# Kernel tuning notes

Hardware: AMD Instinct MI355X
Metric: run time of the kernel (lower is better)

## Reference

```python
import jax, jax.numpy as jnp
import numpy as np

B, S, E, H, W, L = 2048, 50, 256, 512, 256, 50  # batch, seq, emb, hidden, weight, answer_seq_len
V = 50 + 1  # input_size + 1 embedding rows


def _uni(k, shape, bound):
    return jax.random.uniform(k, shape, jnp.float32, -bound, bound)


def setup_inputs() -> dict:
    key = jax.random.key(0)
    ks = jax.random.split(key, 14)
    kb = 1.0 / np.sqrt(H)  # torch LSTM/Linear init bound 1/sqrt(hidden)
    inp = {
        'input': jax.random.randint(ks[0], (B, S), 0, V),
        'emb': jax.random.normal(ks[1], (V, E), jnp.float32),
        'enc_Wih': _uni(ks[2], (4 * H, E), kb),
        'enc_Whh': _uni(ks[3], (4 * H, H), kb),
        'enc_bih': _uni(ks[4], (4 * H,), kb),
        'enc_bhh': _uni(ks[5], (4 * H,), kb),
        'dec_Wih': _uni(ks[6], (4 * H, E), kb),
        'dec_Whh': _uni(ks[7], (4 * H, H), kb),
        'dec_bih': _uni(ks[8], (4 * H,), kb),
        'dec_bhh': _uni(ks[9], (4 * H,), kb),
        'W1': _uni(ks[10], (W, H), kb),
        'W2': _uni(ks[11], (W, H), kb),
        'vt': _uni(ks[12], (W,), 1.0 / np.sqrt(W)),
    }
    return inp


def _lstm_cell(x, h, c, Wih, Whh, bih, bhh):
    gates = x @ Wih.T + h @ Whh.T + (bih + bhh)
    i, f, g, o = jnp.split(gates, 4, axis=-1)  # torch gate order i,f,g,o
    c = jax.nn.sigmoid(f) * c + jax.nn.sigmoid(i) * jnp.tanh(g)
    h = jax.nn.sigmoid(o) * jnp.tanh(c)
    return h, c


def reference(input, emb, enc_Wih, enc_Whh, enc_bih, enc_bhh,
              dec_Wih, dec_Whh, dec_bih, dec_bhh, W1, W2, vt):
    x = emb[input]  # [B,S,E]

    def enc_step(carry, xt):
        h, c = carry
        h, c = _lstm_cell(xt, h, c, enc_Wih, enc_Whh, enc_bih, enc_bhh)
        return (h, c), h

    z = jnp.zeros((B, H), x.dtype)
    _, enc_seq = jax.lax.scan(enc_step, (z, z), x.transpose(1, 0, 2))  # [S,B,H]
    enc_states = enc_seq.transpose(1, 0, 2)  # [B,S,H]

    # W1(encoder_states) is loop-invariant; compute once (same math as per-step recompute)
    blend1 = jnp.einsum('bsh,wh->bsw', enc_states, W1)  # [B,S,W]

    dec_in = jnp.zeros((B, E), x.dtype)  # original never updates decoder_input
    h0 = jnp.zeros((B, H), x.dtype)
    c0 = enc_seq[-1]  # cell_state = encoder_states[-1]
    mask0 = jnp.zeros((B, S), bool)

    def dec_step(carry, k):
        h, c, mask = carry
        h, c = _lstm_cell(dec_in, h, c, dec_Wih, dec_Whh, dec_bih, dec_bhh)
        blend2 = h @ W2.T  # [B,W]
        scores = jnp.einsum('bsw,w->bs', jnp.tanh(blend1 + blend2[:, None, :]), vt)
        scores = jnp.where(mask, jnp.float32(-100000.0), scores)
        logp = jax.nn.log_softmax(scores, axis=-1)  # [B,S]
        chosen = jax.random.categorical(k, logp, axis=-1)  # [B]
        mask = mask.at[jnp.arange(B), chosen].set(True)
        return (h, c, mask), (logp, chosen)

    keys = jax.random.split(jax.random.key(42), L)
    _, (probs, tour) = jax.lax.scan(dec_step, (h0, c0, mask0), keys)
    probs = probs.transpose(1, 0, 2)  # [B,L,S]
    tour = tour.transpose(1, 0)       # [B,L]
    return probs, tour
```

## Files before the change

kernel.cpp:

```cpp
#include <hip/hip_runtime.h>
#include <cstdint>

#define Bsz 2048
#define Ssz 50
#define Esz 256
#define Hsz 512
#define Wsz 256
#define Lsz 50
#define Vsz 51
#define KI 16
#define CH 5
#define GFRAGC2 ((size_t)32 * 128 * 512)

#define JAX_THREEFRY_PARTITIONABLE 1

typedef _Float16 f16;
typedef _Float16 f16x8 __attribute__((ext_vector_type(8)));
typedef float f32x4 __attribute__((ext_vector_type(4)));

__host__ __device__ __forceinline__ void threefry2x32_hd(
    unsigned k0, unsigned k1, unsigned x0, unsigned x1,
    unsigned& o0, unsigned& o1) {
  unsigned ks2 = k0 ^ k1 ^ 0x1BD11BDAu;
  x0 += k0; x1 += k1;
#define TF_RND(r) { x0 += x1; x1 = (x1 << (r)) | (x1 >> (32 - (r))); x1 ^= x0; }
  TF_RND(13) TF_RND(15) TF_RND(26) TF_RND(6)
  x0 += k1; x1 += ks2 + 1u;
  TF_RND(17) TF_RND(29) TF_RND(16) TF_RND(24)
  x0 += ks2; x1 += k0 + 2u;
  TF_RND(13) TF_RND(15) TF_RND(26) TF_RND(6)
  x0 += k0; x1 += k1 + 3u;
  TF_RND(17) TF_RND(29) TF_RND(16) TF_RND(24)
  x0 += k1; x1 += ks2 + 4u;
  TF_RND(13) TF_RND(15) TF_RND(26) TF_RND(6)
  x0 += ks2; x1 += k0 + 5u;
#undef TF_RND
  o0 = x0; o1 = x1;
}

__global__ __launch_bounds__(512) void prep_gfrag(const float* __restrict__ Whh,
                                                  f16* __restrict__ dst) {
  int blk = blockIdx.x;
  int ntile = blk >> 5, kc = blk & 31;
  int t = threadIdx.x;
  int l = t >> 3, e = t & 7;
  int c = l & 15, kg = l >> 4;
  int n = ntile * 16 + c;
  int k = (kc & 15) * 32 + kg * 8 + e;
  int j = n >> 2, g = n & 3;
  float w = Whh[(size_t)(g * 512 + j) * 512 + k];
  f16 hi = (f16)w;
  float lo = w - (float)hi;
  f16 val = (kc < 16) ? hi : (f16)(lo * 2048.0f);
  dst[((size_t)kc * 128 + ntile) * 512 + t] = val;
}

__global__ __launch_bounds__(512) void prep_bfrag(const float* __restrict__ Wm,
                                                  f16* __restrict__ dst) {
  int blk = blockIdx.x;
  int wtile = blk >> 5, kc = blk & 31;
  int t = threadIdx.x;
  int l = t >> 3, e = t & 7;
  int c = l & 15, kg = l >> 4;
  int n = wtile * 16 + c;
  int k = (kc & 15) * 32 + kg * 8 + e;
  float w = Wm[(size_t)n * 512 + k];
  f16 hi = (f16)w;
  float lo = w - (float)hi;
  f16 val = (kc < 16) ? hi : (f16)(lo * 2048.0f);
  dst[((size_t)kc * 16 + wtile) * 512 + t] = val;
}

__global__ __launch_bounds__(256) void prep_encin(
    const float* __restrict__ emb, const float* __restrict__ Wih,
    const float* __restrict__ bih, const float* __restrict__ bhh,
    float* __restrict__ encInP) {
  int wid = blockIdx.x * 4 + (threadIdx.x >> 6);
  int lane = threadIdx.x & 63;
  if (wid >= Vsz * 2048) return;
  int v = wid >> 11, col = wid & 2047;
  float4 e = ((const float4*)emb)[v * 64 + lane];
  float4 w = ((const float4*)Wih)[col * 64 + lane];
  float d = e.x * w.x + e.y * w.y + e.z * w.z + e.w * w.w;
  for (int off = 32; off; off >>= 1) d += __shfl_xor(d, off);
  if (lane == 0) {
    int g = col >> 9, j = col & 511;
    encInP[(size_t)v * 2048 + j * 4 + g] = d + bih[col] + bhh[col];
  }
}

__global__ __launch_bounds__(256) void prep_dbias(const float* __restrict__ a,
                                                  const float* __restrict__ b,
                                                  float* __restrict__ dst) {
  int col = blockIdx.x * 256 + threadIdx.x;
  int g = col >> 9, j = col & 511;
  dst[j * 4 + g] = a[col] + b[col];
}

__global__ __launch_bounds__(256, 2) void gates_mfma(
    const f16* __restrict__ Afrag,
    const f16* __restrict__ Bfrag,
    const float* __restrict__ addtab, const int* __restrict__ input, int tstep,
    f16* __restrict__ Aout,
    float* __restrict__ cio) {
  __shared__ float Cst[64][132];
  const int t = threadIdx.x;
  const int lane = t & 63;
  const int wid = t >> 6;
  const int wm = wid >> 1, wn = wid & 1;
  const int bid = blockIdx.x;
  const int xcd = bid & 7, loc = bid >> 3;
  const int mblk = xcd * 4 + (loc >> 4);
  const int nblk = loc & 15;

  const f16* Ab = Afrag + (size_t)(mblk * 4 + wm * 2) * 512 + lane * 8;
  const f16* Bb = Bfrag + (size_t)(nblk * 8 + wn * 4) * 512 + lane * 8;

  f32x4 acc1[2][4], acc2[2][4];
  {
    f32x4 z = {0.f, 0.f, 0.f, 0.f};
#pragma unroll
    for (int i = 0; i < 2; ++i)
#pragma unroll
      for (int j = 0; j < 4; ++j) { acc1[i][j] = z; acc2[i][j] = z; }
  }

  f16x8 pah[2], pal[2], pbh[4], pbl[4];
  f16x8 qah[2], qal[2], qbh[4], qbl[4];

#define GLOAD(AH_, AL_, BH_, BL_, ki_)                                        \
  {                                                                           \
    const f16* ak = Ab + (size_t)(ki_)*65536;                                 \
    const f16* bk = Bb + (size_t)(ki_)*65536;                                 \
    _Pragma("unroll")                                                         \
    for (int q = 0; q < 2; ++q) {                                             \
      AH_[q] = *(const f16x8*)(ak + q * 512);                                 \
      AL_[q] = *(const f16x8*)(ak + (size_t)16 * 65536 + q * 512);            \
    }                                                                         \
    _Pragma("unroll")                                                         \
    for (int q = 0; q < 4; ++q) {                                             \
      BH_[q] = *(const f16x8*)(bk + q * 512);                                 \
      BL_[q] = *(const f16x8*)(bk + (size_t)16 * 65536 + q * 512);            \
    }                                                                         \
  }
#define GMM(AH_, AL_, BH_, BL_)                                               \
  {                                                                           \
    _Pragma("unroll")                                                         \
    for (int mt = 0; mt < 2; ++mt)                                            \
      _Pragma("unroll")                                                       \
      for (int nt = 0; nt < 4; ++nt)                                          \
        acc1[mt][nt] = __builtin_amdgcn_mfma_f32_16x16x32_f16(                \
            AH_[mt], BH_[nt], acc1[mt][nt], 0, 0, 0);                         \
    _Pragma("unroll")                                                         \
    for (int mt = 0; mt < 2; ++mt)                                            \
      _Pragma("unroll")                                                       \
      for (int nt = 0; nt < 4; ++nt)                                          \
        acc1[mt][nt] = __builtin_amdgcn_mfma_f32_16x16x32_f16(                \
            AL_[mt], BH_[nt], acc1[mt][nt], 0, 0, 0);                         \
    _Pragma("unroll")                                                         \
    for (int mt = 0; mt < 2; ++mt)                                            \
      _Pragma("unroll")                                                       \
      for (int nt = 0; nt < 4; ++nt)                                          \
        acc2[mt][nt] = __builtin_amdgcn_mfma_f32_16x16x32_f16(                \
            AH_[mt], BL_[nt], acc2[mt][nt], 0, 0, 0);                         \
  }

  GLOAD(pah, pal, pbh, pbl, 0)
#pragma unroll 1
  for (int ki = 0; ki < KI; ki += 2) {
    GLOAD(qah, qal, qbh, qbl, ki + 1)
    GMM(pah, pal, pbh, pbl)
    if (ki + 2 < KI) GLOAD(pah, pal, pbh, pbl, ki + 2)
    GMM(qah, qal, qbh, qbl)
  }
#undef GLOAD
#undef GMM

#pragma unroll
  for (int mt = 0; mt < 2; ++mt)
#pragma unroll
    for (int nt = 0; nt < 4; ++nt)
#pragma unroll
      for (int rg = 0; rg < 4; ++rg)
        Cst[wm * 32 + mt * 16 + (lane >> 4) * 4 + rg]
           [wn * 64 + nt * 16 + (lane & 15)] =
            acc1[mt][nt][rg] + acc2[mt][nt][rg] * (1.0f / 2048.0f);
  __syncthreads();

  const int bloc = t & 63, jg = t >> 6;
  const int bg = mblk * 64 + bloc;
  const float* arow = input
      ? addtab + (size_t)input[(size_t)bg * Ssz + tstep] * 2048
      : addtab;

  const int j0 = nblk * 32 + jg * 8;
  float* cp = cio + (size_t)bg * 512 + j0;
  float4 cv0 = *(const float4*)(cp);
  float4 cv1 = *(const float4*)(cp + 4);
  float cin[8] = {cv0.x, cv0.y, cv0.z, cv0.w, cv1.x, cv1.y, cv1.z, cv1.w};
  float cn[8], hv[8];
#pragma unroll
  for (int jj = 0; jj < 8; ++jj) {
    float4 gq = *(const float4*)(&Cst[bloc][jg * 32 + jj * 4]);
    float4 av = *(const float4*)(arow + (size_t)(j0 + jj) * 4);
    float gi = gq.x + av.x;
    float gf = gq.y + av.y;
    float gg = gq.z + av.z;
    float go = gq.w + av.w;
    float si = 1.0f / (1.0f + expf(-gi));
    float sf = 1.0f / (1.0f + expf(-gf));
    float sg = tanhf(gg);
    float so = 1.0f / (1.0f + expf(-go));
    float c2 = sf * cin[jj] + si * sg;
    cn[jj] = c2;
    hv[jj] = so * tanhf(c2);
  }
  *(float4*)(cp)     = make_float4(cn[0], cn[1], cn[2], cn[3]);
  *(float4*)(cp + 4) = make_float4(cn[4], cn[5], cn[6], cn[7]);

  f16x8 hi8, lo8;
#pragma unroll
  for (int jj = 0; jj < 8; ++jj) {
    f16 hi = (f16)hv[jj];
    hi8[jj] = hi;
    lo8[jj] = (f16)(hv[jj] - (float)hi);
  }
  const int kcH = j0 >> 5;
  const int kg = (j0 >> 3) & 3;
  size_t base = (((size_t)kcH * 128 + (bg >> 4)) * 64 + kg * 16 + (bg & 15)) * 8;
  *(f16x8*)(Aout + base)                       = hi8;
  *(f16x8*)(Aout + base + (size_t)16 * 65536)  = lo8;
}

__global__ __launch_bounds__(256) void blend_big(
    const f16* __restrict__ hChunk, const f16* __restrict__ Wb,
    float* __restrict__ outBase, int stepStride, int rowStride) {
  const int t = threadIdx.x, lane = t & 63, wid = t >> 6;
  const int wm = wid >> 1, wn = wid & 1;
  const int bid = blockIdx.x;
  const int nblk = bid / (CH * 32);
  const int mblkG = bid % (CH * 32);
  const int s = mblkG >> 5;
  const int mblkL = mblkG & 31;
  const f16* Ab = hChunk + (size_t)s * GFRAGC2
                + (size_t)(mblkL * 4 + wm * 2) * 512 + lane * 8;
  const f16* Bb = Wb + (size_t)(nblk * 2 + wn) * 512 + lane * 8;

  f32x4 acc1[2], acc2[2];
  {
    f32x4 z = {0.f, 0.f, 0.f, 0.f};
    acc1[0] = z; acc1[1] = z; acc2[0] = z; acc2[1] = z;
  }
  f16x8 pah[2], pal[2], pbh, pbl, qah[2], qal[2], qbh, qbl;

#define BLOAD(AH_, AL_, BH_, BL_, ki_)                                        \
  {                                                                           \
    const f16* ak = Ab + (size_t)(ki_)*65536;                                 \
    const f16* bk = Bb + (size_t)(ki_)*8192;                                  \
    _Pragma("unroll")                                                         \
    for (int q = 0; q < 2; ++q) {                                             \
      AH_[q] = *(const f16x8*)(ak + q * 512);                                 \
      AL_[q] = *(const f16x8*)(ak + (size_t)16 * 65536 + q * 512);            \
    }                                                                         \
    BH_ = *(const f16x8*)(bk);                                                \
    BL_ = *(const f16x8*)(bk + (size_t)16 * 8192);                            \
  }
#define BMM(AH_, AL_, BH_, BL_)                                               \
  {                                                                           \
    _Pragma("unroll")                                                         \
    for (int mt = 0; mt < 2; ++mt)                                            \
      acc1[mt] = __builtin_amdgcn_mfma_f32_16x16x32_f16(                      \
          AH_[mt], BH_, acc1[mt], 0, 0, 0);                                   \
    _Pragma("unroll")                                                         \
    for (int mt = 0; mt < 2; ++mt)                                            \
      acc1[mt] = __builtin_amdgcn_mfma_f32_16x16x32_f16(                      \
          AL_[mt], BH_, acc1[mt], 0, 0, 0);                                   \
    _Pragma("unroll")                                                         \
    for (int mt = 0; mt < 2; ++mt)                                            \
      acc2[mt] = __builtin_amdgcn_mfma_f32_16x16x32_f16(                      \
          AH_[mt], BL_, acc2[mt], 0, 0, 0);                                   \
  }

  BLOAD(pah, pal, pbh, pbl, 0)
#pragma unroll 1
  for (int ki = 0; ki < KI; ki += 2) {
    BLOAD(qah, qal, qbh, qbl, ki + 1)
    BMM(pah, pal, pbh, pbl)
    if (ki + 2 < KI) BLOAD(pah, pal, pbh, pbl, ki + 2)
    BMM(qah, qal, qbh, qbl)
  }
#undef BLOAD
#undef BMM

  const int r = lane & 15, rg4 = (lane >> 4) * 4;
  float* ob = outBase + (size_t)s * stepStride;
#pragma unroll
  for (int mt = 0; mt < 2; ++mt)
#pragma unroll
    for (int rg = 0; rg < 4; ++rg) {
      int b = mblkL * 64 + wm * 32 + mt * 16 + rg4 + rg;
      int w = nblk * 32 + wn * 16 + r;
      ob[(size_t)b * rowStride + w] = acc1[mt][rg] + acc2[mt][rg] * (1.0f / 2048.0f);
    }
}

__global__ __launch_bounds__(256) void dec_cinit(const f16* __restrict__ hE,
                                                 float* __restrict__ cD) {
  int idx = blockIdx.x * 256 + threadIdx.x;
  int b = idx >> 9, j = idx & 511;
  size_t base = (((size_t)(j >> 5) * 128 + (b >> 4)) * 64
                 + ((j >> 3) & 3) * 16 + (b & 15)) * 8 + (j & 7);
  cD[idx] = (float)hE[base] + (float)hE[base + (size_t)16 * 65536];
}

__global__ __launch_bounds__(256) void scores_sample(
    const float* __restrict__ b1, const float* __restrict__ b2,
    const float* __restrict__ vt, unsigned long long* __restrict__ mask,
    float* __restrict__ probs, float* __restrict__ tour,
    int stepk, unsigned kA, unsigned kB) {
  __shared__ float b2s[256];
  __shared__ float vts[256];
  __shared__ float sc[52];
  const int t = threadIdx.x, b = blockIdx.x;
  b2s[t] = b2[(size_t)b * Wsz + t];
  vts[t] = vt[t];
  __syncthreads();
  const int wave = t >> 6, lane = t & 63;
  for (int s = wave; s < Ssz; s += 4) {
    const float* row = b1 + ((size_t)b * Ssz + s) * Wsz;
    float v = 0.f;
#pragma unroll
    for (int q = 0; q < 4; ++q) {
      int w = lane + 64 * q;
      v += vts[w] * tanhf(row[w] + b2s[w]);
    }
    for (int off = 32; off; off >>= 1) v += __shfl_xor(v, off);
    if (lane == 0) sc[s] = v;
  }
  __syncthreads();
  if (wave == 0) {
    unsigned long long m = mask[b];
    float x = (lane < Ssz) ? sc[lane] : -INFINITY;
    if (lane < Ssz && ((m >> lane) & 1ull)) x = -100000.0f;
    float mv = x;
    for (int off = 32; off; off >>= 1) mv = fmaxf(mv, __shfl_xor(mv, off));
    float sh = x - mv;
    float e = (lane < Ssz) ? expf(sh) : 0.f;
    float ssum = e;
    for (int off = 32; off; off >>= 1) ssum += __shfl_xor(ssum, off);
    float lg = logf(ssum);
    float logp = sh - lg;
    if (lane < Ssz) probs[(size_t)b * (Lsz * Ssz) + stepk * Ssz + lane] = logp;

    float val = -INFINITY;
    if (lane < Ssz) {
      unsigned j = (unsigned)(b * Ssz + lane);
      unsigned o0, o1, bits;
#if JAX_THREEFRY_PARTITIONABLE
      threefry2x32_hd(kA, kB, 0u, j, o0, o1);
      bits = o0 ^ o1;
#else
      if (j < 51200u) { threefry2x32_hd(kA, kB, j, j + 51200u, o0, o1); bits = o0; }
      else           { threefry2x32_hd(kA, kB, j - 51200u, j, o0, o1); bits = o1; }
#endif
      float f = __uint_as_float((bits >> 9) | 0x3F800000u) - 1.0f;
      float u = fmaxf(1.17549435e-38f, f + 1.17549435e-38f);
      val = logp - logf(-logf(u));
    }
    int idx = lane;
    for (int off = 32; off; off >>= 1) {
      float ov = __shfl_xor(val, off);
      int oi = __shfl_xor(idx, off);
      if (ov > val || (ov == val && oi < idx)) { val = ov; idx = oi; }
    }
    if (lane == 0) {
      tour[(size_t)b * Lsz + stepk] = (float)idx;
      mask[b] = m | (1ull << idx);
    }
  }
}

extern "C" void kernel_launch(void* const* d_in, const int* in_sizes, int n_in,
                              void* d_out, int out_size, void* d_ws, size_t ws_size,
                              hipStream_t stream) {
  (void)in_sizes; (void)n_in; (void)out_size; (void)ws_size;
  const int*   input = (const int*)d_in[0];
  const float* emb   = (const float*)d_in[1];
  const float* eWih  = (const float*)d_in[2];
  const float* eWhh  = (const float*)d_in[3];
  const float* ebih  = (const float*)d_in[4];
  const float* ebhh  = (const float*)d_in[5];
  const float* dWhh  = (const float*)d_in[7];
  const float* dbih  = (const float*)d_in[8];
  const float* dbhh  = (const float*)d_in[9];
  const float* W1    = (const float*)d_in[10];
  const float* W2    = (const float*)d_in[11];
  const float* vt    = (const float*)d_in[12];
  float* outF = (float*)d_out;

  float* wsf = (float*)d_ws;
  size_t o = 0;
  const size_t BFRAG = (size_t)32 * 16 * 512;
  f16* BfE = (f16*)(wsf + o); o += GFRAGC2 / 2;
  f16* BfD = (f16*)(wsf + o); o += GFRAGC2 / 2;
  f16* Bb1 = (f16*)(wsf + o); o += BFRAG / 2;
  f16* Bb2 = (f16*)(wsf + o); o += BFRAG / 2;
  float* encInP = wsf + o; o += (size_t)Vsz * 2048;
  float* dbiasP = wsf + o; o += 2048;
  f16* hZero = (f16*)(wsf + o); o += GFRAGC2 / 2;
  f16* hBuf  = (f16*)(wsf + o); o += CH * (GFRAGC2 / 2);
  float* cE  = wsf + o; o += (size_t)Bsz * Hsz;
  float* b2c = wsf + o; o += (size_t)CH * Bsz * Wsz;
  float* b1  = wsf + o; o += (size_t)Bsz * Ssz * Wsz;
  unsigned long long* maskp = (unsigned long long*)(wsf + o); o += Bsz * 2;

  hipMemsetAsync(hZero, 0, GFRAGC2 * 2, stream);
  hipMemsetAsync(cE, 0, (size_t)Bsz * Hsz * 4, stream);
  hipMemsetAsync(maskp, 0, (size_t)Bsz * 8, stream);

  prep_gfrag<<<128 * 32, 512, 0, stream>>>(eWhh, BfE);
  prep_gfrag<<<128 * 32, 512, 0, stream>>>(dWhh, BfD);
  prep_bfrag<<<16 * 32, 512, 0, stream>>>(W1, Bb1);
  prep_bfrag<<<16 * 32, 512, 0, stream>>>(W2, Bb2);
  prep_encin<<<(Vsz * 2048) / 4, 256, 0, stream>>>(emb, eWih, ebih, ebhh, encInP);
  prep_dbias<<<8, 256, 0, stream>>>(dbih, dbhh, dbiasP);

  unsigned kAh[Lsz], kBh[Lsz];
  for (int k = 0; k < Lsz; ++k) {
#if JAX_THREEFRY_PARTITIONABLE
    threefry2x32_hd(0u, 42u, 0u, (unsigned)k, kAh[k], kBh[k]);
#else
    unsigned a0, a1, c0, c1;
    if (k < 25) {
      threefry2x32_hd(0u, 42u, 2u * k,      2u * k + 50u, a0, a1); kAh[k] = a0;
      threefry2x32_hd(0u, 42u, 2u * k + 1u, 2u * k + 51u, c0, c1); kBh[k] = c0;
    } else {
      threefry2x32_hd(0u, 42u, 2u * k - 50u, 2u * k,      a0, a1); kAh[k] = a1;
      threefry2x32_hd(0u, 42u, 2u * k - 49u, 2u * k + 1u, c0, c1); kBh[k] = c1;
    }
#endif
  }

  const size_t GF = GFRAGC2;

  for (int c = 0; c < Ssz / CH; ++c) {
    for (int s = 0; s < CH; ++s) {
      int t = c * CH + s;
      const f16* in = (t == 0) ? hZero : hBuf + (size_t)((t - 1) % CH) * GF;
      gates_mfma<<<512, 256, 0, stream>>>(in, BfE, encInP, input, t,
                                          hBuf + (size_t)s * GF, cE);
    }
    blend_big<<<8 * CH * 32, 256, 0, stream>>>(hBuf, Bb1,
                                               b1 + (size_t)(c * CH) * Wsz,
                                               Wsz, Ssz * Wsz);
  }
  dec_cinit<<<(Bsz * Hsz) / 256, 256, 0, stream>>>(
      hBuf + (size_t)((Ssz - 1) % CH) * GF, cE);

  for (int c = 0; c < Lsz / CH; ++c) {
    for (int s = 0; s < CH; ++s) {
      int k = c * CH + s;
      const f16* in = (k == 0) ? hZero : hBuf + (size_t)((k - 1) % CH) * GF;
      gates_mfma<<<512, 256, 0, stream>>>(in, BfD, dbiasP, nullptr, 0,
                                          hBuf + (size_t)s * GF, cE);
    }
    blend_big<<<8 * CH * 32, 256, 0, stream>>>(hBuf, Bb2, b2c,
                                               Bsz * Wsz, Wsz);
    for (int s = 0; s < CH; ++s) {
      int k = c * CH + s;
      scores_sample<<<Bsz, 256, 0, stream>>>(b1, b2c + (size_t)s * Bsz * Wsz,
                                             vt, maskp, outF,
                                             outF + (size_t)Bsz * Lsz * Ssz,
                                             k, kAh[k], kBh[k]);
    }
  }
}
```

Measured before the change: 3.923 ms.

## Fuse per-step sampling into chunked kernel with LDS-cached blend1, enlarge chunk

Replaces the per-step scores_sample launches with one sample_chunk kernel per chunk. It loads each batch row's blend1 (50x256 floats, 51 KB) into LDS once and loops over the chunk's decode steps, keeping the mask in a register and computing the threefry step keys on device. CH doubles from 5 to 10, halving the blend_big launches and growing the workspace buffers. blend_big's block index mapping is reordered so blocks sharing an M-tile land on the same XCD. The large LDS allocation limits occupancy of the sampling kernel.

```diff
diff --git a/kernel.cpp b/kernel.cpp
--- a/kernel.cpp
+++ b/kernel.cpp
@@ -9,7 +9,7 @@
 #define Lsz 50
 #define Vsz 51
 #define KI 16
-#define CH 5
+#define CH 10
 #define GFRAGC2 ((size_t)32 * 128 * 512)
 
 #define JAX_THREEFRY_PARTITIONABLE 1
@@ -238,10 +238,13 @@
   const int t = threadIdx.x, lane = t & 63, wid = t >> 6;
   const int wm = wid >> 1, wn = wid & 1;
   const int bid = blockIdx.x;
-  const int nblk = bid / (CH * 32);
-  const int mblkG = bid % (CH * 32);
-  const int s = mblkG >> 5;
-  const int mblkL = mblkG & 31;
+  const int xcd = bid & 7;
+  const int r1 = bid >> 3;
+  const int nblk = r1 & 7;
+  const int r2 = r1 >> 3;
+  const int mrem = r2 & 3;
+  const int s = r2 >> 2;
+  const int mblkL = xcd * 4 + mrem;
   const f16* Ab = hChunk + (size_t)s * GFRAGC2
                 + (size_t)(mblkL * 4 + wm * 2) * 512 + lane * 8;
   const f16* Bb = Wb + (size_t)(nblk * 2 + wn) * 512 + lane * 8;
@@ -313,71 +316,96 @@
   cD[idx] = (float)hE[base] + (float)hE[base + (size_t)16 * 65536];
 }
 
-__global__ __launch_bounds__(256) void scores_sample(
-    const float* __restrict__ b1, const float* __restrict__ b2,
+__global__ __launch_bounds__(256) void sample_chunk(
+    const float* __restrict__ b1, const float* __restrict__ b2c,
     const float* __restrict__ vt, unsigned long long* __restrict__ mask,
-    float* __restrict__ probs, float* __restrict__ tour,
-    int stepk, unsigned kA, unsigned kB) {
-  __shared__ float b2s[256];
-  __shared__ float vts[256];
+    float* __restrict__ probs, float* __restrict__ tour, int k0) {
+  __shared__ float b1s[Ssz * Wsz];
+  __shared__ float b2s[Wsz];
+  __shared__ float vts[Wsz];
   __shared__ float sc[52];
   const int t = threadIdx.x, b = blockIdx.x;
-  b2s[t] = b2[(size_t)b * Wsz + t];
   vts[t] = vt[t];
-  __syncthreads();
+  {
+    const float4* src = (const float4*)(b1 + (size_t)b * Ssz * Wsz);
+    for (int i = t; i < (Ssz * Wsz) / 4; i += 256)
+      ((float4*)b1s)[i] = src[i];
+  }
+  unsigned long long m = mask[b];
   const int wave = t >> 6, lane = t & 63;
-  for (int s = wave; s < Ssz; s += 4) {
-    const float* row = b1 + ((size_t)b * Ssz + s) * Wsz;
-    float v = 0.f;
-#pragma unroll
-    for (int q = 0; q < 4; ++q) {
-      int w = lane + 64 * q;
-      v += vts[w] * tanhf(row[w] + b2s[w]);
+
+  for (int kk = 0; kk < CH; ++kk) {
+    const int stepk = k0 + kk;
+    __syncthreads();
+    b2s[t] = b2c[((size_t)kk * Bsz + b) * Wsz + t];
+    __syncthreads();
+    for (int s = wave; s < Ssz; s += 4) {
+      const float* row = b1s + s * Wsz;
+      float v = 0.f;
+#pragma unroll
+      for (int q = 0; q < 4; ++q) {
+        int w = lane + 64 * q;
+        v += vts[w] * tanhf(row[w] + b2s[w]);
+      }
+      for (int off = 32; off; off >>= 1) v += __shfl_xor(v, off);
+      if (lane == 0) sc[s] = v;
     }
-    for (int off = 32; off; off >>= 1) v += __shfl_xor(v, off);
-    if (lane == 0) sc[s] = v;
-  }
-  __syncthreads();
-  if (wave == 0) {
-    unsigned long long m = mask[b];
-    float x = (lane < Ssz) ? sc[lane] : -INFINITY;
-    if (lane < Ssz && ((m >> lane) & 1ull)) x = -100000.0f;
-    float mv = x;
-    for (int off = 32; off; off >>= 1) mv = fmaxf(mv, __shfl_xor(mv, off));
-    float sh = x - mv;
-    float e = (lane < Ssz) ? expf(sh) : 0.f;
-    float ssum = e;
-    for (int off = 32; off; off >>= 1) ssum += __shfl_xor(ssum, off);
-    float lg = logf(ssum);
-    float logp = sh - lg;
-    if (lane < Ssz) probs[(size_t)b * (Lsz * Ssz) + stepk * Ssz + lane] = logp;
-
-    float val = -INFINITY;
-    if (lane < Ssz) {
-      unsigned j = (unsigned)(b * Ssz + lane);
-      unsigned o0, o1, bits;
+    __syncthreads();
+    if (wave == 0) {
+      float x = (lane < Ssz) ? sc[lane] : -INFINITY;
+      if (lane < Ssz && ((m >> lane) & 1ull)) x = -100000.0f;
+      float mv = x;
+      for (int off = 32; off; off >>= 1) mv = fmaxf(mv, __shfl_xor(mv, off));
+      float sh = x - mv;
+      float e = (lane < Ssz) ? expf(sh) : 0.f;
+      float ssum = e;
+      for (int off = 32; off; off >>= 1) ssum += __shfl_xor(ssum, off);
+      float lg = logf(ssum);
+      float logp = sh - lg;
+      if (lane < Ssz) probs[(size_t)b * (Lsz * Ssz) + stepk * Ssz + lane] = logp;
+
+      unsigned kA, kB;
 #if JAX_THREEFRY_PARTITIONABLE
-      threefry2x32_hd(kA, kB, 0u, j, o0, o1);
-      bits = o0 ^ o1;
+      threefry2x32_hd(0u, 42u, 0u, (unsigned)stepk, kA, kB);
 #else
-      if (j < 51200u) { threefry2x32_hd(kA, kB, j, j + 51200u, o0, o1); bits = o0; }
-      else           { threefry2x32_hd(kA, kB, j - 51200u, j, o0, o1); bits = o1; }
+      {
+        unsigned a0, a1, c0, c1;
+        int k = stepk;
+        if (k < 25) {
+          threefry2x32_hd(0u, 42u, 2u * k,      2u * k + 50u, a0, a1); kA = a0;
+          threefry2x32_hd(0u, 42u, 2u * k + 1u, 2u * k + 51u, c0, c1); kB = c0;
+        } else {
+          threefry2x32_hd(0u, 42u, 2u * k - 50u, 2u * k,      a0, a1); kA = a1;
+          threefry2x32_hd(0u, 42u, 2u * k - 49u, 2u * k + 1u, c0, c1); kB = c1;
+        }
+      }
 #endif
-      float f = __uint_as_float((bits >> 9) | 0x3F800000u) - 1.0f;
-      float u = fmaxf(1.17549435e-38f, f + 1.17549435e-38f);
-      val = logp - logf(-logf(u));
+      float val = -INFINITY;
+      if (lane < Ssz) {
+        unsigned j = (unsigned)(b * Ssz + lane);
+        unsigned o0, o1, bits;
+#if JAX_THREEFRY_PARTITIONABLE
+        threefry2x32_hd(kA, kB, 0u, j, o0, o1);
+        bits = o0 ^ o1;
+#else
+        if (j < 51200u) { threefry2x32_hd(kA, kB, j, j + 51200u, o0, o1); bits = o0; }
+        else           { threefry2x32_hd(kA, kB, j - 51200u, j, o0, o1); bits = o1; }
+#endif
+        float f = __uint_as_float((bits >> 9) | 0x3F800000u) - 1.0f;
+        float u = fmaxf(1.17549435e-38f, f + 1.17549435e-38f);
+        val = logp - logf(-logf(u));
+      }
+      int idx = lane;
+      for (int off = 32; off; off >>= 1) {
+        float ov = __shfl_xor(val, off);
+        int oi = __shfl_xor(idx, off);
+        if (ov > val || (ov == val && oi < idx)) { val = ov; idx = oi; }
+      }
+      if (lane == 0) tour[(size_t)b * Lsz + stepk] = (float)idx;
+      m |= (1ull << idx);
     }
-    int idx = lane;
-    for (int off = 32; off; off >>= 1) {
-      float ov = __shfl_xor(val, off);
-      int oi = __shfl_xor(idx, off);
-      if (ov > val || (ov == val && oi < idx)) { val = ov; idx = oi; }
-    }
-    if (lane == 0) {
-      tour[(size_t)b * Lsz + stepk] = (float)idx;
-      mask[b] = m | (1ull << idx);
-    }
-  }
+  }
+  if (t == 0) mask[b] = m;
 }
 
 extern "C" void kernel_launch(void* const* d_in, const int* in_sizes, int n_in,
@@ -425,22 +453,6 @@
   prep_encin<<<(Vsz * 2048) / 4, 256, 0, stream>>>(emb, eWih, ebih, ebhh, encInP);
   prep_dbias<<<8, 256, 0, stream>>>(dbih, dbhh, dbiasP);
 
-  unsigned kAh[Lsz], kBh[Lsz];
-  for (int k = 0; k < Lsz; ++k) {
-#if JAX_THREEFRY_PARTITIONABLE
-    threefry2x32_hd(0u, 42u, 0u, (unsigned)k, kAh[k], kBh[k]);
-#else
-    unsigned a0, a1, c0, c1;
-    if (k < 25) {
-      threefry2x32_hd(0u, 42u, 2u * k,      2u * k + 50u, a0, a1); kAh[k] = a0;
-      threefry2x32_hd(0u, 42u, 2u * k + 1u, 2u * k + 51u, c0, c1); kBh[k] = c0;
-    } else {
-      threefry2x32_hd(0u, 42u, 2u * k - 50u, 2u * k,      a0, a1); kAh[k] = a1;
-      threefry2x32_hd(0u, 42u, 2u * k - 49u, 2u * k + 1u, c0, c1); kBh[k] = c1;
-    }
-#endif
-  }
-
   const size_t GF = GFRAGC2;
 
   for (int c = 0; c < Ssz / CH; ++c) {
@@ -450,9 +462,9 @@
       gates_mfma<<<512, 256, 0, stream>>>(in, BfE, encInP, input, t,
                                           hBuf + (size_t)s * GF, cE);
     }
-    blend_big<<<8 * CH * 32, 256, 0, stream>>>(hBuf, Bb1,
-                                               b1 + (size_t)(c * CH) * Wsz,
-                                               Wsz, Ssz * Wsz);
+    blend_big<<<8 * 8 * 4 * CH, 256, 0, stream>>>(hBuf, Bb1,
+                                                  b1 + (size_t)(c * CH) * Wsz,
+                                                  Wsz, Ssz * Wsz);
   }
   dec_cinit<<<(Bsz * Hsz) / 256, 256, 0, stream>>>(
       hBuf + (size_t)((Ssz - 1) % CH) * GF, cE);
@@ -464,14 +476,10 @@
       gates_mfma<<<512, 256, 0, stream>>>(in, BfD, dbiasP, nullptr, 0,
                                           hBuf + (size_t)s * GF, cE);
     }
-    blend_big<<<8 * CH * 32, 256, 0, stream>>>(hBuf, Bb2, b2c,
-                                               Bsz * Wsz, Wsz);
-    for (int s = 0; s < CH; ++s) {
-      int k = c * CH + s;
-      scores_sample<<<Bsz, 256, 0, stream>>>(b1, b2c + (size_t)s * Bsz * Wsz,
-                                             vt, maskp, outF,
-                                             outF + (size_t)Bsz * Lsz * Ssz,
-                                             k, kAh[k], kBh[k]);
-    }
-  }
-}
+    blend_big<<<8 * 8 * 4 * CH, 256, 0, stream>>>(hBuf, Bb2, b2c,
+                                                  Bsz * Wsz, Wsz);
+    sample_chunk<<<Bsz, 256, 0, stream>>>(b1, b2c, vt, maskp, outF,
+                                          outF + (size_t)Bsz * Lsz * Ssz,
+                                          c * CH);
+  }
+}
```

Result: no change. 3.940 ms (+0.4%).
